# Kernel tuning notes

Hardware: AMD Instinct MI355X
Metric: run time of the kernel (lower is better)

Reference implementation:

```python
import jax, jax.numpy as jnp
import numpy as np

B, L, D_LLM, C_OH, D = 256, 128, 1024, 64, 256
HEADS, LAYERS, EDGE_DIM, NET, E_PER = 4, 4, 64, 8, 256
N = B * L
DH = D // HEADS


def _layer_norm(x, g, b, eps=1e-5):
    m = x.mean(-1, keepdims=True)
    v = ((x - m) ** 2).mean(-1, keepdims=True)
    return (x - m) / jnp.sqrt(v + eps) * g + b


def _conv(h, src, dst, ea, Wq, bq, Wk, bk, Wv, bv, We, Ws, bs, Wb):
    # PyG TransformerConv (concat=True, beta=True, edge_dim): per-edge gather of Q(dst), K/V(src)
    q = (h @ Wq + bq)[dst].reshape(-1, HEADS, DH)
    k = (h @ Wk + bk)[src].reshape(-1, HEADS, DH)
    v = (h @ Wv + bv)[src].reshape(-1, HEADS, DH)
    e = (ea @ We).reshape(-1, HEADS, DH)
    k = k + e
    v = v + e
    alpha = (q * k).sum(-1) / jnp.sqrt(jnp.float32(DH))  # [E, H]
    amax = jax.ops.segment_max(alpha, dst, num_segments=N)  # segment softmax over dst
    ex = jnp.exp(alpha - amax[dst])
    den = jax.ops.segment_sum(ex, dst, num_segments=N)
    a = ex / den[dst]
    out = jax.ops.segment_sum(a[:, :, None] * v, dst, num_segments=N).reshape(N, D)
    xr = h @ Ws + bs  # root/skip projection
    beta = jax.nn.sigmoid(jnp.concatenate([out, xr, out - xr], axis=-1) @ Wb)  # [N,1]
    return beta * xr + (1.0 - beta) * out


def _gnorm(x, batch, w, b, ms, eps=1e-5):
    # PyG GraphNorm: per-graph mean with learnable mean_scale, per-graph variance
    cnt = jax.ops.segment_sum(jnp.ones((N,), x.dtype), batch, num_segments=B)[:, None]
    mean = jax.ops.segment_sum(x, batch, num_segments=B) / cnt
    out = x - mean[batch] * ms
    var = jax.ops.segment_sum(out * out, batch, num_segments=B) / cnt
    return w * out / jnp.sqrt(var + eps)[batch] + b


def _forward(atom_llm, atom_onehot, mask, edge_index, edge_type, batch,
             ln_llm_g, ln_llm_b, W_llm, b_llm, W_oh, edge_emb, edge_ln_g, edge_ln_b,
             Wq, bq, Wk, bk, Wv, bv, We, Ws, bs, Wb, gn_w, gn_b, gn_ms,
             W1, b1, W2, b2, out_ln_g, out_ln_b):
    x = (_layer_norm(atom_llm, ln_llm_g, ln_llm_b) @ W_llm + b_llm) + atom_onehot @ W_oh
    x = x * mask[..., None]
    h = x.reshape(N, D)  # all graphs full length L -> packing == reshape
    ea = _layer_norm(edge_emb[edge_type], edge_ln_g, edge_ln_b)
    src, dst = edge_index[0], edge_index[1]
    for l in range(LAYERS):
        h2 = _conv(h, src, dst, ea, Wq[l], bq[l], Wk[l], bk[l], Wv[l], bv[l], We[l], Ws[l], bs[l], Wb[l])
        h = _gnorm(h + h2, batch, gn_w[l], gn_b[l], gn_ms[l])
        h = jax.nn.gelu(h, approximate=False)
    ff = jax.nn.gelu(h @ W1 + b1, approximate=False) @ W2 + b2
    h = _layer_norm(h + ff, out_ln_g, out_ln_b)
    return h.reshape(B, L, D) * mask[..., None]


def setup_inputs():
    key = jax.random.key(0)
    ks = jax.random.split(key, 64)
    rng = np.random.default_rng(0)
    atom_llm = jax.random.normal(ks[0], (B, L, D_LLM), jnp.float32)
    atom_onehot = jax.random.uniform(ks[1], (B, L, C_OH), jnp.float32)
    mask = jnp.ones((B, L), jnp.float32)
    # per-graph random edges u != v, global offsets, undirected doubling
    u = rng.integers(0, L, size=(B, E_PER))
    v = (u + rng.integers(1, L, size=(B, E_PER))) % L
    et = rng.integers(0, NET, size=(B, E_PER)).reshape(-1)
    off = (np.arange(B) * L)[:, None]
    s = (u + off).reshape(-1)
    d = (v + off).reshape(-1)
    edge_index = jnp.asarray(np.stack([np.concatenate([s, d]), np.concatenate([d, s])]), jnp.int32)
    edge_type = jnp.asarray(np.concatenate([et, et]), jnp.int32)
    batch = jnp.repeat(jnp.arange(B, dtype=jnp.int32), L)

    def lin(k, i, o):
        s = 1.0 / np.sqrt(i)
        return jax.random.uniform(k, (i, o), jnp.float32, -s, s)

    st = lambda f, keys: jnp.stack([f(k) for k in keys])
    kq = jax.random.split(ks[10], LAYERS); kk = jax.random.split(ks[11], LAYERS)
    kv = jax.random.split(ks[12], LAYERS); ke = jax.random.split(ks[13], LAYERS)
    ksk = jax.random.split(ks[14], LAYERS); kb = jax.random.split(ks[15], LAYERS)
    return dict(
        atom_llm=atom_llm, atom_onehot=atom_onehot, mask=mask,
        edge_index=edge_index, edge_type=edge_type, batch=batch,
        ln_llm_g=jnp.ones((D_LLM,)), ln_llm_b=jnp.zeros((D_LLM,)),
        W_llm=lin(ks[2], D_LLM, D), b_llm=jnp.zeros((D,)),
        W_oh=lin(ks[3], C_OH, D),
        edge_emb=jax.random.normal(ks[4], (NET, EDGE_DIM), jnp.float32),
        edge_ln_g=jnp.ones((EDGE_DIM,)), edge_ln_b=jnp.zeros((EDGE_DIM,)),
        Wq=st(lambda k: lin(k, D, D), kq), bq=jnp.zeros((LAYERS, D)),
        Wk=st(lambda k: lin(k, D, D), kk), bk=jnp.zeros((LAYERS, D)),
        Wv=st(lambda k: lin(k, D, D), kv), bv=jnp.zeros((LAYERS, D)),
        We=st(lambda k: lin(k, EDGE_DIM, D), ke),
        Ws=st(lambda k: lin(k, D, D), ksk), bs=jnp.zeros((LAYERS, D)),
        Wb=st(lambda k: lin(k, 3 * D, 1), kb),
        gn_w=jnp.ones((LAYERS, D)), gn_b=jnp.zeros((LAYERS, D)), gn_ms=jnp.ones((LAYERS, D)),
        W1=lin(ks[6], D, 4 * D) * 0.5, b1=jnp.zeros((4 * D,)),
        W2=lin(ks[7], 4 * D, D) * 0.5, b2=jnp.zeros((D,)),
        out_ln_g=jnp.ones((D,)), out_ln_b=jnp.zeros((D,)),
    )


def reference(atom_llm, atom_onehot, mask, edge_index, edge_type, batch,
              ln_llm_g, ln_llm_b, W_llm, b_llm, W_oh, edge_emb, edge_ln_g, edge_ln_b,
              Wq, bq, Wk, bk, Wv, bv, We, Ws, bs, Wb, gn_w, gn_b, gn_ms,
              W1, b1, W2, b2, out_ln_g, out_ln_b):
    return _forward(atom_llm, atom_onehot, mask, edge_index, edge_type, batch,
                    ln_llm_g, ln_llm_b, W_llm, b_llm, W_oh, edge_emb, edge_ln_g, edge_ln_b,
                    Wq, bq, Wk, bk, Wv, bv, We, Ws, bs, Wb, gn_w, gn_b, gn_ms,
                    W1, b1, W2, b2, out_ln_g, out_ln_b)
```

## Files before the change

### kernel.cpp

```cpp
#include <hip/hip_runtime.h>
#include <math.h>

#define NB      256
#define LL      128
#define NN      32768
#define DLLM    1024
#define COH     64
#define DD      256
#define NLAYERS 4
#define EDIM    64
#define NETT    8
#define NE      131072
#define CHUNK   16

typedef unsigned short bf16_t;
typedef __bf16 bf16x8 __attribute__((ext_vector_type(8)));
typedef float f32x4v __attribute__((ext_vector_type(4)));

__device__ __forceinline__ float bf2f(bf16_t u){
    return __uint_as_float(((unsigned int)u) << 16);
}
__device__ __forceinline__ bf16_t f2bf(float f){
    unsigned int x = __float_as_uint(f);
    return (bf16_t)((x + 0x7fffu + ((x >> 16) & 1u)) >> 16);
}
__device__ __forceinline__ unsigned pack2(float a, float b){
    return (unsigned)f2bf(a) | ((unsigned)f2bf(b) << 16);
}
__device__ __forceinline__ float gelu_exact(float x){
    return 0.5f * x * (1.0f + erff(x * 0.70710678118654752440f));
}
__device__ __forceinline__ float wave_reduce_sum(float v){
#pragma unroll
    for (int off = 32; off; off >>= 1) v += __shfl_xor(v, off);
    return v;
}

__global__ void zero_kernel(int* __restrict__ p, int n){
    int i = blockIdx.x * blockDim.x + threadIdx.x;
    if (i < n) p[i] = 0;
}

__global__ __launch_bounds__(256)
void ln_concat_kernel(const float* __restrict__ A, const float* __restrict__ onehot,
                      const float* __restrict__ g, const float* __restrict__ b,
                      bf16_t* __restrict__ xln){
    int wave = threadIdx.x >> 6, lane = threadIdx.x & 63;
    int row = (blockIdx.x << 2) + wave;
    const float* p = A + (size_t)row * DLLM;
    float4 v[4];
    float s = 0.f, sq = 0.f;
#pragma unroll
    for (int c = 0; c < 4; c++){
        v[c] = *(const float4*)(p + c * 256 + (lane << 2));
        s  += v[c].x + v[c].y + v[c].z + v[c].w;
        sq += v[c].x*v[c].x + v[c].y*v[c].y + v[c].z*v[c].z + v[c].w*v[c].w;
    }
    s = wave_reduce_sum(s); sq = wave_reduce_sum(sq);
    float mean = s * (1.0f / DLLM);
    float var  = sq * (1.0f / DLLM) - mean * mean;
    float rstd = rsqrtf(var + 1e-5f);
    bf16_t* out = xln + (size_t)row * 1088;
#pragma unroll
    for (int c = 0; c < 4; c++){
        float4 g4 = *(const float4*)(g + c * 256 + (lane << 2));
        float4 b4 = *(const float4*)(b + c * 256 + (lane << 2));
        float rx = (v[c].x - mean) * rstd * g4.x + b4.x;
        float ry = (v[c].y - mean) * rstd * g4.y + b4.y;
        float rz = (v[c].z - mean) * rstd * g4.z + b4.z;
        float rw = (v[c].w - mean) * rstd * g4.w + b4.w;
        ushort4 u; u.x = f2bf(rx); u.y = f2bf(ry); u.z = f2bf(rz); u.w = f2bf(rw);
        *(ushort4*)(out + c * 256 + (lane << 2)) = u;
    }
    out[1024 + lane] = f2bf(onehot[(size_t)row * COH + lane]);
}

__global__ __launch_bounds__(256)
void edgeproj_kernel(const float* __restrict__ edge_emb,
                     const float* __restrict__ lg, const float* __restrict__ lb,
                     const float* __restrict__ We, float* __restrict__ eproj){
    int l = blockIdx.x >> 3, t = blockIdx.x & 7;
    __shared__ float ea[EDIM];
    int tid = threadIdx.x;
    if (tid < 64){
        float v = edge_emb[t * EDIM + tid];
        float s = v, sq = v * v;
#pragma unroll
        for (int off = 32; off; off >>= 1){ s += __shfl_xor(s, off); sq += __shfl_xor(sq, off); }
        float mean = s * (1.f/64.f);
        float var  = sq * (1.f/64.f) - mean * mean;
        float rstd = rsqrtf(var + 1e-5f);
        ea[tid] = (v - mean) * rstd * lg[tid] + lb[tid];
    }
    __syncthreads();
    const float* W = We + (size_t)l * EDIM * DD;
    float s = 0.f;
#pragma unroll
    for (int k = 0; k < EDIM; k++) s += ea[k] * W[k * DD + tid];
    eproj[((l << 3) + t) * DD + tid] = s;
}

__global__ void count_kernel(const int* __restrict__ dst, int* __restrict__ cnt){
    int e = blockIdx.x * blockDim.x + threadIdx.x;
    if (e < NE){
        int d = dst[e];
        if (d >= 0 && d < NN) atomicAdd(&cnt[d], 1);
    }
}

__global__ __launch_bounds__(1024)
void scan_kernel(const int* __restrict__ cnt, int* __restrict__ rowstart, int* __restrict__ cursor){
    __shared__ int sh[1024];
    int tid = threadIdx.x;
    int carry = 0;
    for (int base = 0; base < NN; base += 1024){
        int v = cnt[base + tid];
        sh[tid] = v; __syncthreads();
        for (int off = 1; off < 1024; off <<= 1){
            int t = (tid >= off) ? sh[tid - off] : 0;
            __syncthreads();
            sh[tid] += t;
            __syncthreads();
        }
        int excl = carry + sh[tid] - v;
        rowstart[base + tid] = excl;
        cursor[base + tid]   = excl;
        carry += sh[1023];
        __syncthreads();
    }
    if (tid == 0) rowstart[NN] = carry;
}

__global__ void scatter_kernel(const int* __restrict__ dst, const int* __restrict__ src,
                               const int* __restrict__ etype, int* __restrict__ cursor,
                               int* __restrict__ epack){
    int e = blockIdx.x * blockDim.x + threadIdx.x;
    if (e < NE){
        int d = dst[e];
        if (d >= 0 && d < NN){
            int p = atomicAdd(&cursor[d], 1);
            if (p >= 0 && p < NE){
                int sv = src[e]; if (sv < 0 || sv >= NN) sv = 0;
                epack[p] = ((sv & 127) << 3) | (etype[e] & 7);
            }
        }
    }
}

__global__ void wcvt_in_kernel(const float* __restrict__ Wllm, const float* __restrict__ Woh,
                               bf16_t* __restrict__ dst){
    int idx = blockIdx.x * blockDim.x + threadIdx.x;
    if (idx >= 256 * 1088) return;
    int n = idx / 1088, k = idx % 1088;
    float v = (k < 1024) ? Wllm[(size_t)k * 256 + n] : Woh[(size_t)(k - 1024) * 256 + n];
    dst[idx] = f2bf(v);
}

__global__ void wcvt_qkvs_kernel(const float* __restrict__ Wq, const float* __restrict__ Wk,
                                 const float* __restrict__ Wv, const float* __restrict__ Ws,
                                 bf16_t* __restrict__ dst){
    int idx = blockIdx.x * blockDim.x + threadIdx.x;
    if (idx >= NLAYERS * 1024 * 256) return;
    int l = idx >> 18, rem = idx & 262143;
    int n = rem >> 8, k = rem & 255;
    int sel = n >> 8, nn = n & 255;
    const float* W = (sel == 0) ? Wq : (sel == 1) ? Wk : (sel == 2) ? Wv : Ws;
    dst[idx] = f2bf(W[(size_t)l * 65536 + (size_t)k * 256 + nn]);
}

__global__ void wcvt_w1_kernel(const float* __restrict__ W1, bf16_t* __restrict__ dst){
    int idx = blockIdx.x * blockDim.x + threadIdx.x;
    if (idx >= 1024 * 256) return;
    int n = idx >> 8, k = idx & 255;
    dst[idx] = f2bf(W1[(size_t)k * 1024 + n]);
}

__global__ void wcvt_w2_kernel(const float* __restrict__ W2, bf16_t* __restrict__ dst){
    int idx = blockIdx.x * blockDim.x + threadIdx.x;
    if (idx >= 256 * 1024) return;
    int n = idx >> 10, k = idx & 1023;
    dst[idx] = f2bf(W2[(size_t)k * 256 + n]);
}

__global__ void pack_bias_kernel(const float* __restrict__ bq, const float* __restrict__ bk,
                                 const float* __restrict__ bv, const float* __restrict__ bs,
                                 float* __restrict__ dst){
    int idx = blockIdx.x * blockDim.x + threadIdx.x;
    if (idx >= NLAYERS * 1024) return;
    int l = idx >> 10, n = idx & 1023;
    int sel = n >> 8, nn = n & 255;
    const float* B = (sel == 0) ? bq : (sel == 1) ? bk : (sel == 2) ? bv : bs;
    dst[idx] = B[l * 256 + nn];
}

template<bool A_F32, bool HAS_BIAS, bool GELU_EP, bool MASK_EP, bool WRITE_F32, bool WRITE_BF16>
__global__ __launch_bounds__(256)
void mfma_gemm(const void* __restrict__ Av, const bf16_t* __restrict__ BT,
               float* __restrict__ Cf, bf16_t* __restrict__ Cb,
               int Ncols, int K,
               const float* __restrict__ bias, const float* __restrict__ mask)
{
    __shared__ bf16_t As[128][40];
    __shared__ bf16_t Bs[128][40];
    const int tid  = threadIdx.x;
    const int rowBase = blockIdx.y << 7;
    const int colBase = blockIdx.x << 7;
    const int lane = tid & 63;
    const int wave = tid >> 6;
    const int wm = wave >> 1, wn = wave & 1;
    const int lhi = lane >> 4, llo = lane & 15;
    const int r0 = tid >> 2;
    const int q0 = (tid & 3) << 3;

    f32x4v acc[4][4];
#pragma unroll
    for (int m = 0; m < 4; m++)
#pragma unroll
        for (int n = 0; n < 4; n++)
            acc[m][n] = (f32x4v){0.f, 0.f, 0.f, 0.f};

    const int nk = K >> 5;
    for (int ks = 0; ks < nk; ks++){
        const int k0 = ks << 5;
        if constexpr (A_F32){
            const float* Ap = (const float*)Av;
#pragma unroll
            for (int half = 0; half < 2; half++){
                int r = r0 + half * 64;
                const float* p = Ap + (size_t)(rowBase + r) * K + (k0 + q0);
                float4 a = *(const float4*)p;
                float4 b = *(const float4*)(p + 4);
                uint4 pk;
                pk.x = pack2(a.x, a.y); pk.y = pack2(a.z, a.w);
                pk.z = pack2(b.x, b.y); pk.w = pack2(b.z, b.w);
                *(uint4*)&As[r][q0] = pk;
            }
        } else {
            const bf16_t* Ap = (const bf16_t*)Av;
#pragma unroll
            for (int half = 0; half < 2; half++){
                int r = r0 + half * 64;
                *(uint4*)&As[r][q0] = *(const uint4*)(Ap + (size_t)(rowBase + r) * K + (k0 + q0));
            }
        }
#pragma unroll
        for (int half = 0; half < 2; half++){
            int r = r0 + half * 64;
            *(uint4*)&Bs[r][q0] = *(const uint4*)(BT + (size_t)(colBase + r) * K + (k0 + q0));
        }
        __syncthreads();
        bf16x8 af[4], bfr[4];
#pragma unroll
        for (int m = 0; m < 4; m++)
            af[m] = *(const bf16x8*)&As[(wm << 6) + (m << 4) + llo][lhi << 3];
#pragma unroll
        for (int n = 0; n < 4; n++)
            bfr[n] = *(const bf16x8*)&Bs[(wn << 6) + (n << 4) + llo][lhi << 3];
#pragma unroll
        for (int m = 0; m < 4; m++)
#pragma unroll
            for (int n = 0; n < 4; n++)
                acc[m][n] = __builtin_amdgcn_mfma_f32_16x16x32_bf16(af[m], bfr[n], acc[m][n], 0, 0, 0);
        __syncthreads();
    }

#pragma unroll
    for (int m = 0; m < 4; m++){
        const int rowb = rowBase + (wm << 6) + (m << 4) + (lhi << 2);
#pragma unroll
        for (int n = 0; n < 4; n++){
            const int col = colBase + (wn << 6) + (n << 4) + llo;
            float bv = 0.f;
            if constexpr (HAS_BIAS) bv = bias[col];
#pragma unroll
            for (int r = 0; r < 4; r++){
                float v = acc[m][n][r] + bv;
                if constexpr (GELU_EP) v = gelu_exact(v);
                if constexpr (MASK_EP) v *= mask[rowb + r];
                if constexpr (WRITE_F32) Cf[(size_t)(rowb + r) * Ncols + col] = v;
                if constexpr (WRITE_BF16) Cb[(size_t)(rowb + r) * Ncols + col] = f2bf(v);
            }
        }
    }
}

__global__ __launch_bounds__(512)
void attn_graph_kernel(const bf16_t* __restrict__ QKVS, const float* __restrict__ h,
                       const int* __restrict__ rowstart, const int* __restrict__ epack,
                       const float* __restrict__ eproj, const float* __restrict__ Wb,
                       float* __restrict__ S)
{
    __shared__ bf16_t Kl[128][256];
    __shared__ bf16_t Vl[128][256];
    __shared__ float  epl[8][256];
    __shared__ float  al[8][CHUNK][4];
    const int g = blockIdx.x;
    const int tid = threadIdx.x;
    const int wave = tid >> 6, lane = tid & 63;
    const int hgrp = lane >> 4;
    const int d4 = lane << 2;
    const size_t gbase = (size_t)g * 128 * 1024;

    for (int i = tid; i < 128 * 32; i += 512){
        int n = i >> 5, c = (i & 31) << 3;
        *(uint4*)&Kl[n][c] = *(const uint4*)(QKVS + gbase + (size_t)n * 1024 + 256 + c);
        *(uint4*)&Vl[n][c] = *(const uint4*)(QKVS + gbase + (size_t)n * 1024 + 512 + c);
    }
    for (int i = tid; i < 8 * 256; i += 512) epl[i >> 8][i & 255] = eproj[i];
    __syncthreads();

    float4 w0 = *(const float4*)(Wb + d4);
    float4 w1 = *(const float4*)(Wb + 256 + d4);
    float4 w2 = *(const float4*)(Wb + 512 + d4);

    for (int ni = 0; ni < 16; ni++){
        int nl = (wave << 4) + ni;
        int node = (g << 7) + nl;
        int s0 = rowstart[node];
        int deg = rowstart[node + 1] - s0;
        if (deg < 0) deg = 0;
        ushort4 qu = *(const ushort4*)(QKVS + gbase + (size_t)nl * 1024 + d4);
        float q0 = bf2f(qu.x), q1 = bf2f(qu.y), q2 = bf2f(qu.z), q3 = bf2f(qu.w);
        float m = -1e30f, den = 0.f;
        float v0 = 0.f, v1 = 0.f, v2 = 0.f, v3 = 0.f;
        for (int c0 = 0; c0 < deg; c0 += CHUNK){
            int ce = deg - c0; if (ce > CHUNK) ce = CHUNK;
            for (int i = 0; i < ce; i++){
                int pk = epack[s0 + c0 + i];
                int sl = pk >> 3, t = pk & 7;
                ushort4 ku = *(const ushort4*)&Kl[sl][d4];
                float4 ev = *(const float4*)&epl[t][d4];
                float d = q0 * (bf2f(ku.x) + ev.x) + q1 * (bf2f(ku.y) + ev.y)
                        + q2 * (bf2f(ku.z) + ev.z) + q3 * (bf2f(ku.w) + ev.w);
                d += __shfl_xor(d, 1); d += __shfl_xor(d, 2);
                d += __shfl_xor(d, 4); d += __shfl_xor(d, 8);
                if ((lane & 15) == 0) al[wave][i][hgrp] = d * 0.125f;
            }
            float cm = -1e30f;
            for (int i = 0; i < ce; i++) cm = fmaxf(cm, al[wave][i][hgrp]);
            float mnew = fmaxf(m, cm);
            float scale = expf(m - mnew);
            den *= scale; v0 *= scale; v1 *= scale; v2 *= scale; v3 *= scale;
            for (int i = 0; i < ce; i++){
                int pk = epack[s0 + c0 + i];
                int sl = pk >> 3, t = pk & 7;
                float w = expf(al[wave][i][hgrp] - mnew);
                den += w;
                ushort4 vu = *(const ushort4*)&Vl[sl][d4];
                float4 ev = *(const float4*)&epl[t][d4];
                v0 = fmaf(w, bf2f(vu.x) + ev.x, v0);
                v1 = fmaf(w, bf2f(vu.y) + ev.y, v1);
                v2 = fmaf(w, bf2f(vu.z) + ev.z, v2);
                v3 = fmaf(w, bf2f(vu.w) + ev.w, v3);
            }
            m = mnew;
        }
        float inv = (den > 0.f) ? 1.f / den : 0.f;
        v0 *= inv; v1 *= inv; v2 *= inv; v3 *= inv;
        ushort4 xu = *(const ushort4*)(QKVS + gbase + (size_t)nl * 1024 + 768 + d4);
        float x0 = bf2f(xu.x), x1 = bf2f(xu.y), x2 = bf2f(xu.z), x3 = bf2f(xu.w);
        float part = v0*w0.x + v1*w0.y + v2*w0.z + v3*w0.w
                   + x0*w1.x + x1*w1.y + x2*w1.z + x3*w1.w
                   + (v0-x0)*w2.x + (v1-x1)*w2.y + (v2-x2)*w2.z + (v3-x3)*w2.w;
        part = wave_reduce_sum(part);
        float beta = 1.f / (1.f + expf(-part));
        float4 hv = *(const float4*)(h + ((size_t)node << 8) + d4);
        float4 r;
        r.x = hv.x + beta * x0 + (1.f - beta) * v0;
        r.y = hv.y + beta * x1 + (1.f - beta) * v1;
        r.z = hv.z + beta * x2 + (1.f - beta) * v2;
        r.w = hv.w + beta * x3 + (1.f - beta) * v3;
        *(float4*)(S + ((size_t)node << 8) + d4) = r;
    }
}

__global__ __launch_bounds__(256)
void graphnorm_gelu_kernel(const float* __restrict__ xin, const float* __restrict__ w,
                           const float* __restrict__ b, const float* __restrict__ ms,
                           float* __restrict__ hout)
{
    int g = blockIdx.x, d = threadIdx.x;
    const float* base = xin + (size_t)g * LL * DD + d;
    float s = 0.f;
    for (int n = 0; n < LL; n++) s += base[n * DD];
    float sub = s * (1.f / LL) * ms[d];
    float var = 0.f;
    for (int n = 0; n < LL; n++){ float t = base[n * DD] - sub; var += t * t; }
    var *= (1.f / LL);
    float rs = rsqrtf(var + 1e-5f);
    float wd = w[d], bd = b[d];
    float* ob = hout + (size_t)g * LL * DD + d;
    for (int n = 0; n < LL; n++){
        float t = (base[n * DD] - sub) * rs * wd + bd;
        ob[n * DD] = gelu_exact(t);
    }
}

__global__ __launch_bounds__(256)
void final_ln_kernel(const float* __restrict__ h, const float* __restrict__ ff,
                     const float* __restrict__ g, const float* __restrict__ b,
                     const float* __restrict__ mask, float* __restrict__ outp)
{
    int wave = threadIdx.x >> 6, lane = threadIdx.x & 63;
    int node = (blockIdx.x << 2) + wave;
    int d0 = lane << 2;
    float4 hv = *(const float4*)(h  + (size_t)node * DD + d0);
    float4 fv = *(const float4*)(ff + (size_t)node * DD + d0);
    float4 v; v.x = hv.x + fv.x; v.y = hv.y + fv.y; v.z = hv.z + fv.z; v.w = hv.w + fv.w;
    float s  = v.x + v.y + v.z + v.w;
    float sq = v.x*v.x + v.y*v.y + v.z*v.z + v.w*v.w;
    s = wave_reduce_sum(s); sq = wave_reduce_sum(sq);
    float mean = s * (1.f / DD);
    float var  = sq * (1.f / DD) - mean * mean;
    float rs = rsqrtf(var + 1e-5f);
    float mk = mask[node];
    float4 g4 = *(const float4*)(g + d0), b4 = *(const float4*)(b + d0);
    float4 r;
    r.x = ((v.x - mean) * rs * g4.x + b4.x) * mk;
    r.y = ((v.y - mean) * rs * g4.y + b4.y) * mk;
    r.z = ((v.z - mean) * rs * g4.z + b4.z) * mk;
    r.w = ((v.w - mean) * rs * g4.w + b4.w) * mk;
    *(float4*)(outp + (size_t)node * DD + d0) = r;
}

extern "C" void kernel_launch(void* const* d_in, const int* in_sizes, int n_in,
                              void* d_out, int out_size, void* d_ws, size_t ws_size,
                              hipStream_t stream)
{
    if (n_in < 33) return;
    if (in_sizes[0] != NN * DLLM) return;
    if (in_sizes[3] != 2 * NE) return;
    if (in_sizes[8] != DLLM * DD) return;
    if (in_sizes[27] != DD * 4 * DD) return;
    if (out_size != NN * DD) return;

    const float* atom_llm    = (const float*)d_in[0];
    const float* atom_onehot = (const float*)d_in[1];
    const float* mask        = (const float*)d_in[2];
    const int*   edge_index  = (const int*)d_in[3];
    const int*   etype       = (const int*)d_in[4];
    const float* ln_llm_g    = (const float*)d_in[6];
    const float* ln_llm_b    = (const float*)d_in[7];
    const float* W_llm       = (const float*)d_in[8];
    const float* b_llm       = (const float*)d_in[9];
    const float* W_oh        = (const float*)d_in[10];
    const float* edge_emb    = (const float*)d_in[11];
    const float* edge_ln_g   = (const float*)d_in[12];
    const float* edge_ln_b   = (const float*)d_in[13];
    const float* Wq          = (const float*)d_in[14];
    const float* bq          = (const float*)d_in[15];
    const float* Wk          = (const float*)d_in[16];
    const float* bk          = (const float*)d_in[17];
    const float* Wv          = (const float*)d_in[18];
    const float* bv          = (const float*)d_in[19];
    const float* We          = (const float*)d_in[20];
    const float* Ws          = (const float*)d_in[21];
    const float* bs          = (const float*)d_in[22];
    const float* Wb          = (const float*)d_in[23];
    const float* gn_w        = (const float*)d_in[24];
    const float* gn_b        = (const float*)d_in[25];
    const float* gn_ms       = (const float*)d_in[26];
    const float* W1          = (const float*)d_in[27];
    const float* b1          = (const float*)d_in[28];
    const float* W2          = (const float*)d_in[29];
    const float* b2          = (const float*)d_in[30];
    const float* out_ln_g    = (const float*)d_in[31];
    const float* out_ln_b    = (const float*)d_in[32];

    const int* srcv = edge_index;
    const int* dstv = edge_index + NE;

    char* ws = (char*)d_ws;
    size_t off = 0;
    auto alloc = [&](size_t bytes) -> char* {
        char* p = ws + off; off += (bytes + 255) / 256 * 256; return p;
    };
    float*  h    = (float*)alloc((size_t)NN * DD * sizeof(float));
    bf16_t* reg3 = (bf16_t*)alloc((size_t)NN * 1088 * sizeof(bf16_t));
    bf16_t* wt_in   = (bf16_t*)alloc((size_t)256 * 1088 * sizeof(bf16_t));
    bf16_t* wt_qkvs = (bf16_t*)alloc((size_t)NLAYERS * 1024 * 256 * sizeof(bf16_t));
    bf16_t* wt_w1   = (bf16_t*)alloc((size_t)1024 * 256 * sizeof(bf16_t));
    bf16_t* wt_w2   = (bf16_t*)alloc((size_t)256 * 1024 * sizeof(bf16_t));
    float*  biasp   = (float*)alloc((size_t)NLAYERS * 1024 * sizeof(float));
    float*  eproj   = (float*)alloc((size_t)NLAYERS * NETT * DD * sizeof(float));
    int* cnt      = (int*)alloc((size_t)NN * sizeof(int));
    int* rowstart = (int*)alloc((size_t)(NN + 1) * sizeof(int));
    int* cursor   = (int*)alloc((size_t)NN * sizeof(int));
    int* epack    = (int*)alloc((size_t)NE * sizeof(int));
    bf16_t* xln  = reg3;
    bf16_t* qkvs = reg3;
    bf16_t* t1   = reg3;
    float*  S    = (float*)d_out;

    if (ws_size < off) return;

    zero_kernel<<<NN / 256, 256, 0, stream>>>(cnt, NN);
    count_kernel<<<NE / 256, 256, 0, stream>>>(dstv, cnt);
    scan_kernel<<<1, 1024, 0, stream>>>(cnt, rowstart, cursor);
    scatter_kernel<<<NE / 256, 256, 0, stream>>>(dstv, srcv, etype, cursor, epack);

    ln_concat_kernel<<<NN / 4, 256, 0, stream>>>(atom_llm, atom_onehot, ln_llm_g, ln_llm_b, xln);
    edgeproj_kernel<<<NLAYERS * NETT, 256, 0, stream>>>(edge_emb, edge_ln_g, edge_ln_b, We, eproj);
    wcvt_in_kernel<<<(256 * 1088 + 255) / 256, 256, 0, stream>>>(W_llm, W_oh, wt_in);
    wcvt_qkvs_kernel<<<(NLAYERS * 1024 * 256) / 256, 256, 0, stream>>>(Wq, Wk, Wv, Ws, wt_qkvs);
    wcvt_w1_kernel<<<(1024 * 256) / 256, 256, 0, stream>>>(W1, wt_w1);
    wcvt_w2_kernel<<<(256 * 1024) / 256, 256, 0, stream>>>(W2, wt_w2);
    pack_bias_kernel<<<(NLAYERS * 1024) / 256, 256, 0, stream>>>(bq, bk, bv, bs, biasp);

    {
        dim3 grid(DD / 128, NN / 128);
        mfma_gemm<false, true, false, true, true, false><<<grid, 256, 0, stream>>>(
            xln, wt_in, h, nullptr, DD, 1088, b_llm, mask);
    }

    for (int l = 0; l < NLAYERS; l++){
        dim3 grid(1024 / 128, NN / 128);
        mfma_gemm<true, true, false, false, false, true><<<grid, 256, 0, stream>>>(
            h, wt_qkvs + (size_t)l * 1024 * 256, nullptr, qkvs, 1024, DD,
            biasp + (size_t)l * 1024, nullptr);

        attn_graph_kernel<<<NB, 512, 0, stream>>>(qkvs, h, rowstart, epack,
                                                  eproj + (size_t)l * NETT * DD,
                                                  Wb + (size_t)l * 768, S);

        graphnorm_gelu_kernel<<<NB, 256, 0, stream>>>(S, gn_w + l * DD, gn_b + l * DD,
                                                      gn_ms + l * DD, h);
    }

    {
        dim3 grid1(1024 / 128, NN / 128);
        mfma_gemm<true, true, true, false, false, true><<<grid1, 256, 0, stream>>>(
            h, wt_w1, nullptr, t1, 1024, DD, b1, nullptr);
        dim3 grid2(DD / 128, NN / 128);
        mfma_gemm<false, true, false, false, true, false><<<grid2, 256, 0, stream>>>(
            t1, wt_w2, S, nullptr, DD, 1024, b2, nullptr);
        final_ln_kernel<<<NN / 4, 256, 0, stream>>>(h, S, out_ln_g, out_ln_b, mask,
                                                    (float*)d_out);
    }
}
```

Baseline: 1.130 ms.

## Fuse graph attention with GraphNorm+GELU and read K/V directly from global memory

```diff
diff --git a/kernel.cpp b/kernel.cpp
--- a/kernel.cpp
+++ b/kernel.cpp
@@ -11,7 +11,6 @@
 #define EDIM    64
 #define NETT    8
 #define NE      131072
-#define CHUNK   16
 
 typedef unsigned short bf16_t;
 typedef __bf16 bf16x8 __attribute__((ext_vector_type(8)));
@@ -284,80 +283,91 @@
     }
 }
 
-__global__ __launch_bounds__(512)
-void attn_graph_kernel(const bf16_t* __restrict__ QKVS, const float* __restrict__ h,
+__global__ __launch_bounds__(1024)
+void attn_gnorm_kernel(const bf16_t* __restrict__ QKVS, float* __restrict__ h,
                        const int* __restrict__ rowstart, const int* __restrict__ epack,
                        const float* __restrict__ eproj, const float* __restrict__ Wb,
-                       float* __restrict__ S)
+                       const float* __restrict__ gw, const float* __restrict__ gb,
+                       const float* __restrict__ gms)
 {
-    __shared__ bf16_t Kl[128][256];
-    __shared__ bf16_t Vl[128][256];
-    __shared__ float  epl[8][256];
-    __shared__ float  al[8][CHUNK][4];
+    __shared__ float epl[8][256];
+    __shared__ float gsumL[16][256];
+    __shared__ float gsqL[16][256];
+    __shared__ float msubL[256], rswL[256], gbL[256];
     const int g = blockIdx.x;
     const int tid = threadIdx.x;
     const int wave = tid >> 6, lane = tid & 63;
-    const int hgrp = lane >> 4;
     const int d4 = lane << 2;
-    const size_t gbase = (size_t)g * 128 * 1024;
-
-    for (int i = tid; i < 128 * 32; i += 512){
-        int n = i >> 5, c = (i & 31) << 3;
-        *(uint4*)&Kl[n][c] = *(const uint4*)(QKVS + gbase + (size_t)n * 1024 + 256 + c);
-        *(uint4*)&Vl[n][c] = *(const uint4*)(QKVS + gbase + (size_t)n * 1024 + 512 + c);
-    }
-    for (int i = tid; i < 8 * 256; i += 512) epl[i >> 8][i & 255] = eproj[i];
+    const size_t gbase = (size_t)g << 17;
+
+    for (int i = tid; i < 2048; i += 1024) epl[i >> 8][i & 255] = eproj[i];
     __syncthreads();
 
     float4 w0 = *(const float4*)(Wb + d4);
     float4 w1 = *(const float4*)(Wb + 256 + d4);
     float4 w2 = *(const float4*)(Wb + 512 + d4);
 
-    for (int ni = 0; ni < 16; ni++){
-        int nl = (wave << 4) + ni;
-        int node = (g << 7) + nl;
+    float Sreg[8][4];
+    float gs0 = 0.f, gs1 = 0.f, gs2 = 0.f, gs3 = 0.f;
+    float gq0 = 0.f, gq1 = 0.f, gq2 = 0.f, gq3 = 0.f;
+
+#pragma unroll
+    for (int ni = 0; ni < 8; ni++){
+        const int nl = (wave << 3) + ni;
+        const int node = (g << 7) + nl;
         int s0 = rowstart[node];
         int deg = rowstart[node + 1] - s0;
         if (deg < 0) deg = 0;
-        ushort4 qu = *(const ushort4*)(QKVS + gbase + (size_t)nl * 1024 + d4);
+        ushort4 qu = *(const ushort4*)(QKVS + gbase + ((size_t)nl << 10) + d4);
         float q0 = bf2f(qu.x), q1 = bf2f(qu.y), q2 = bf2f(qu.z), q3 = bf2f(qu.w);
         float m = -1e30f, den = 0.f;
         float v0 = 0.f, v1 = 0.f, v2 = 0.f, v3 = 0.f;
-        for (int c0 = 0; c0 < deg; c0 += CHUNK){
-            int ce = deg - c0; if (ce > CHUNK) ce = CHUNK;
-            for (int i = 0; i < ce; i++){
-                int pk = epack[s0 + c0 + i];
-                int sl = pk >> 3, t = pk & 7;
-                ushort4 ku = *(const ushort4*)&Kl[sl][d4];
-                float4 ev = *(const float4*)&epl[t][d4];
-                float d = q0 * (bf2f(ku.x) + ev.x) + q1 * (bf2f(ku.y) + ev.y)
-                        + q2 * (bf2f(ku.z) + ev.z) + q3 * (bf2f(ku.w) + ev.w);
-                d += __shfl_xor(d, 1); d += __shfl_xor(d, 2);
-                d += __shfl_xor(d, 4); d += __shfl_xor(d, 8);
-                if ((lane & 15) == 0) al[wave][i][hgrp] = d * 0.125f;
+        for (int c0 = 0; c0 < deg; c0 += 8){
+            int ce = deg - c0; if (ce > 8) ce = 8;
+            int pk[8]; float pa[8];
+#pragma unroll
+            for (int i = 0; i < 8; i++)
+                pk[i] = (i < ce) ? epack[s0 + c0 + i] : 0;
+#pragma unroll
+            for (int i = 0; i < 8; i++){
+                if (i < ce){
+                    int sl = pk[i] >> 3, t = pk[i] & 7;
+                    ushort4 ku = *(const ushort4*)(QKVS + gbase + ((size_t)sl << 10) + 256 + d4);
+                    float4 ev = *(const float4*)&epl[t][d4];
+                    float d = q0 * (bf2f(ku.x) + ev.x) + q1 * (bf2f(ku.y) + ev.y)
+                            + q2 * (bf2f(ku.z) + ev.z) + q3 * (bf2f(ku.w) + ev.w);
+                    d += __shfl_xor(d, 1); d += __shfl_xor(d, 2);
+                    d += __shfl_xor(d, 4); d += __shfl_xor(d, 8);
+                    pa[i] = d * 0.125f;
+                } else {
+                    pa[i] = -1e30f;
+                }
             }
-            float cm = -1e30f;
-            for (int i = 0; i < ce; i++) cm = fmaxf(cm, al[wave][i][hgrp]);
+            float cm = pa[0];
+#pragma unroll
+            for (int i = 1; i < 8; i++) cm = fmaxf(cm, pa[i]);
             float mnew = fmaxf(m, cm);
             float scale = expf(m - mnew);
             den *= scale; v0 *= scale; v1 *= scale; v2 *= scale; v3 *= scale;
-            for (int i = 0; i < ce; i++){
-                int pk = epack[s0 + c0 + i];
-                int sl = pk >> 3, t = pk & 7;
-                float w = expf(al[wave][i][hgrp] - mnew);
-                den += w;
-                ushort4 vu = *(const ushort4*)&Vl[sl][d4];
-                float4 ev = *(const float4*)&epl[t][d4];
-                v0 = fmaf(w, bf2f(vu.x) + ev.x, v0);
-                v1 = fmaf(w, bf2f(vu.y) + ev.y, v1);
-                v2 = fmaf(w, bf2f(vu.z) + ev.z, v2);
-                v3 = fmaf(w, bf2f(vu.w) + ev.w, v3);
+#pragma unroll
+            for (int i = 0; i < 8; i++){
+                if (i < ce){
+                    int sl = pk[i] >> 3, t = pk[i] & 7;
+                    float w = expf(pa[i] - mnew);
+                    den += w;
+                    ushort4 vu = *(const ushort4*)(QKVS + gbase + ((size_t)sl << 10) + 512 + d4);
+                    float4 ev = *(const float4*)&epl[t][d4];
+                    v0 = fmaf(w, bf2f(vu.x) + ev.x, v0);
+                    v1 = fmaf(w, bf2f(vu.y) + ev.y, v1);
+                    v2 = fmaf(w, bf2f(vu.z) + ev.z, v2);
+                    v3 = fmaf(w, bf2f(vu.w) + ev.w, v3);
+                }
             }
             m = mnew;
         }
         float inv = (den > 0.f) ? 1.f / den : 0.f;
         v0 *= inv; v1 *= inv; v2 *= inv; v3 *= inv;
-        ushort4 xu = *(const ushort4*)(QKVS + gbase + (size_t)nl * 1024 + 768 + d4);
+        ushort4 xu = *(const ushort4*)(QKVS + gbase + ((size_t)nl << 10) + 768 + d4);
         float x0 = bf2f(xu.x), x1 = bf2f(xu.y), x2 = bf2f(xu.z), x3 = bf2f(xu.w);
         float part = v0*w0.x + v1*w0.y + v2*w0.z + v3*w0.w
                    + x0*w1.x + x1*w1.y + x2*w1.z + x3*w1.w
@@ -365,34 +375,44 @@
         part = wave_reduce_sum(part);
         float beta = 1.f / (1.f + expf(-part));
         float4 hv = *(const float4*)(h + ((size_t)node << 8) + d4);
+        float r0v = hv.x + beta * x0 + (1.f - beta) * v0;
+        float r1v = hv.y + beta * x1 + (1.f - beta) * v1;
+        float r2v = hv.z + beta * x2 + (1.f - beta) * v2;
+        float r3v = hv.w + beta * x3 + (1.f - beta) * v3;
+        Sreg[ni][0] = r0v; Sreg[ni][1] = r1v; Sreg[ni][2] = r2v; Sreg[ni][3] = r3v;
+        gs0 += r0v; gs1 += r1v; gs2 += r2v; gs3 += r3v;
+        gq0 = fmaf(r0v, r0v, gq0); gq1 = fmaf(r1v, r1v, gq1);
+        gq2 = fmaf(r2v, r2v, gq2); gq3 = fmaf(r3v, r3v, gq3);
+    }
+
+    *(float4*)&gsumL[wave][d4] = make_float4(gs0, gs1, gs2, gs3);
+    *(float4*)&gsqL[wave][d4]  = make_float4(gq0, gq1, gq2, gq3);
+    __syncthreads();
+    if (tid < 256){
+        float s = 0.f, sq = 0.f;
+#pragma unroll
+        for (int j = 0; j < 16; j++){ s += gsumL[j][tid]; sq += gsqL[j][tid]; }
+        float mean = s * (1.f / 128.f);
+        float msub = mean * gms[tid];
+        float var = sq * (1.f / 128.f) - 2.f * msub * mean + msub * msub;
+        float rs = rsqrtf(var + 1e-5f);
+        msubL[tid] = msub;
+        rswL[tid]  = rs * gw[tid];
+        gbL[tid]   = gb[tid];
+    }
+    __syncthreads();
+    float4 ms4 = *(const float4*)&msubL[d4];
+    float4 rw4 = *(const float4*)&rswL[d4];
+    float4 gb4 = *(const float4*)&gbL[d4];
+#pragma unroll
+    for (int ni = 0; ni < 8; ni++){
+        const int node = (g << 7) + (wave << 3) + ni;
         float4 r;
-        r.x = hv.x + beta * x0 + (1.f - beta) * v0;
-        r.y = hv.y + beta * x1 + (1.f - beta) * v1;
-        r.z = hv.z + beta * x2 + (1.f - beta) * v2;
-        r.w = hv.w + beta * x3 + (1.f - beta) * v3;
-        *(float4*)(S + ((size_t)node << 8) + d4) = r;
-    }
-}
-
-__global__ __launch_bounds__(256)
-void graphnorm_gelu_kernel(const float* __restrict__ xin, const float* __restrict__ w,
-                           const float* __restrict__ b, const float* __restrict__ ms,
-                           float* __restrict__ hout)
-{
-    int g = blockIdx.x, d = threadIdx.x;
-    const float* base = xin + (size_t)g * LL * DD + d;
-    float s = 0.f;
-    for (int n = 0; n < LL; n++) s += base[n * DD];
-    float sub = s * (1.f / LL) * ms[d];
-    float var = 0.f;
-    for (int n = 0; n < LL; n++){ float t = base[n * DD] - sub; var += t * t; }
-    var *= (1.f / LL);
-    float rs = rsqrtf(var + 1e-5f);
-    float wd = w[d], bd = b[d];
-    float* ob = hout + (size_t)g * LL * DD + d;
-    for (int n = 0; n < LL; n++){
-        float t = (base[n * DD] - sub) * rs * wd + bd;
-        ob[n * DD] = gelu_exact(t);
+        r.x = gelu_exact((Sreg[ni][0] - ms4.x) * rw4.x + gb4.x);
+        r.y = gelu_exact((Sreg[ni][1] - ms4.y) * rw4.y + gb4.y);
+        r.z = gelu_exact((Sreg[ni][2] - ms4.z) * rw4.z + gb4.z);
+        r.w = gelu_exact((Sreg[ni][3] - ms4.w) * rw4.w + gb4.w);
+        *(float4*)(h + ((size_t)node << 8) + d4) = r;
     }
 }
 
@@ -519,12 +539,10 @@
             h, wt_qkvs + (size_t)l * 1024 * 256, nullptr, qkvs, 1024, DD,
             biasp + (size_t)l * 1024, nullptr);
 
-        attn_graph_kernel<<<NB, 512, 0, stream>>>(qkvs, h, rowstart, epack,
-                                                  eproj + (size_t)l * NETT * DD,
-                                                  Wb + (size_t)l * 768, S);
-
-        graphnorm_gelu_kernel<<<NB, 256, 0, stream>>>(S, gn_w + l * DD, gn_b + l * DD,
-                                                      gn_ms + l * DD, h);
+        attn_gnorm_kernel<<<NB, 1024, 0, stream>>>(qkvs, h, rowstart, epack,
+                                                   eproj + (size_t)l * NETT * DD,
+                                                   Wb + (size_t)l * 768,
+                                                   gn_w + l * DD, gn_b + l * DD, gn_ms + l * DD);
     }
 
     {
```

Result: faster. 1.078 ms (-4.6%).
